# Kernel optimization log

Hardware: AMD Instinct MI355X
Metric: run time of the kernel (lower is better)

Reference implementation:

```python
import jax, jax.numpy as jnp
import numpy as np

B, N, K = 2, 8192, 9
IN_CH, FEAT_CH, COST_CH = 64, 128, 64

def _bn(x, p, eps=1e-5):
    # eval-mode BatchNorm; p is [4, C] = (gamma, beta, running_mean, running_var)
    sh = (1, -1) + (1,) * (x.ndim - 2)
    g, b, m, v = (p[i].reshape(sh) for i in range(4))
    return (x - m) / jnp.sqrt(v + eps) * g + b

def _c1(x, w, b):
    # Conv1d kernel 1: x [B,C,N], w [O,C]
    return jnp.einsum('oc,bcn->bon', w, x) + b[None, :, None]

def _forward(xyz, points, cost_volume, feats, flow,
             w0, b0, bn0, w1, b1, bn1,
             wz, bz, wr, br, wq, bq,
             w2a, b2a, w2b, b2b, wfc, bfc,
             rw0, rbn0, rw1, rbn1, rw2, rbn2,
             cw0, cbn0, cw1, cbn1, cw2, cbn2):
    lrelu = lambda t: jax.nn.leaky_relu(t, 0.1)
    # --- self-KNN on xyz ---
    xt = jnp.transpose(xyz, (0, 2, 1))                   # B N 3
    sq = jnp.sum(xt * xt, -1)                            # B N
    d2 = sq[:, :, None] + sq[:, None, :] - 2.0 * jnp.einsum('bnd,bmd->bnm', xt, xt)
    idx = jax.lax.top_k(-d2, K)[1]                       # B N K (nearest incl. self)
    # --- grouping_operation: gather neighbor features ---
    np0 = jnp.concatenate([cost_volume, flow], 1)        # B (cost_ch+3) N
    g = jax.vmap(lambda p, i: p[:, i])(np0, idx)         # B C N K
    # --- Conv2d(1x1)+BN+LeakyReLU stack ---
    g = lrelu(_bn(jnp.einsum('oc,bcnk->bonk', w0, g) + b0[None, :, None, None], bn0))
    g = lrelu(_bn(jnp.einsum('oc,bcnk->bonk', w1, g) + b1[None, :, None, None], bn1))
    h = jnp.max(g, -1)                                   # max over neighbors -> B 128 N
    # --- ConvGRU(x=feats, h) with 1x1 Conv1d gates ---
    hx = jnp.concatenate([h, feats], 1)
    z = jax.nn.sigmoid(_c1(hx, wz, bz))
    r = jax.nn.sigmoid(_c1(hx, wr, br))
    q = jnp.tanh(_c1(jnp.concatenate([r * h, feats], 1), wq, bq))
    h = (1.0 - z) * h + z * q
    # --- Conv1d MLP head ---
    x = jnp.concatenate([points, h], 1)                  # B (in_ch+128) N
    x = lrelu(_c1(x, w2a, b2a))
    x = lrelu(_c1(x, w2b, b2b))
    re_flow = _c1(x, wfc, bfc)                           # B 3 N
    # --- prob regnets (Conv1d no-bias + BN + ReLU) ---
    def reg(y, ws, ps):
        for w, p in zip(ws, ps):
            y = jax.nn.relu(_bn(jnp.einsum('oc,bcn->bon', w, y), p))
        return y
    refine = reg(x, [rw0, rw1, rw2], [rbn0, rbn1, rbn2])         # B 1 N
    coarse = reg(cost_volume, [cw0, cw1, cw2], [cbn0, cbn1, cbn2])
    re_flow = coarse * flow + refine * re_flow
    return x, jnp.clip(re_flow, -20.0, 20.0)

def setup_inputs():
    key = jax.random.key(0)
    ks = iter(jax.random.split(key, 80))
    nrm = lambda shape, s=1.0: jax.random.normal(next(ks), shape, jnp.float32) * s
    def bnp(C):
        g = jax.random.uniform(next(ks), (C,), jnp.float32) + 0.5
        b = nrm((C,), 0.1); m = nrm((C,), 0.1)
        v = jax.random.uniform(next(ks), (C,), jnp.float32) + 0.5
        return jnp.stack([g, b, m, v])
    z = lambda C: jnp.zeros((C,), jnp.float32)
    return dict(
        xyz=nrm((B, 3, N)), points=nrm((B, IN_CH, N)), cost_volume=nrm((B, COST_CH, N)),
        feats=nrm((B, FEAT_CH, N)), flow=nrm((B, 3, N), 0.1),
        w0=nrm((128, COST_CH + 3), 0.05), b0=z(128), bn0=bnp(128),
        w1=nrm((128, 128), 0.05), b1=z(128), bn1=bnp(128),
        wz=nrm((128, 256), 0.05), bz=z(128), wr=nrm((128, 256), 0.05), br=z(128),
        wq=nrm((128, 256), 0.05), bq=z(128),
        w2a=nrm((128, IN_CH + 128), 0.05), b2a=z(128), w2b=nrm((64, 128), 0.05), b2b=z(64),
        wfc=nrm((3, 64), 0.05), bfc=z(3),
        rw0=nrm((64, 64), 0.05), rbn0=bnp(64), rw1=nrm((64, 64), 0.05), rbn1=bnp(64),
        rw2=nrm((1, 64), 0.05), rbn2=bnp(1),
        cw0=nrm((64, COST_CH), 0.05), cbn0=bnp(64), cw1=nrm((64, 64), 0.05), cbn1=bnp(64),
        cw2=nrm((1, 64), 0.05), cbn2=bnp(1),
    )

def reference(xyz, points, cost_volume, feats, flow, w0, b0, bn0, w1, b1, bn1, wz, bz, wr, br, wq, bq, w2a, b2a, w2b, b2b, wfc, bfc, rw0, rbn0, rw1, rbn1, rw2, rbn2, cw0, cbn0, cw1, cbn1, cw2, cbn2):
    return _forward(xyz, points, cost_volume, feats, flow, w0, b0, bn0, w1, b1, bn1, wz, bz, wr, br, wq, bq, w2a, b2a, w2b, b2b, wfc, bfc, rw0, rbn0, rw1, rbn1, rw2, rbn2, cw0, cbn0, cw1, cbn1, cw2, cbn2)
```

## Files before the change

### kernel.cpp

```cpp
#include <hip/hip_runtime.h>
#include <math.h>

typedef __bf16 bf16;
typedef __bf16 bf16x4 __attribute__((ext_vector_type(4)));
typedef __bf16 bf16x8 __attribute__((ext_vector_type(8)));
typedef float f32x4 __attribute__((ext_vector_type(4)));

#define NPTS 8192
#define MTOT 16384

static __device__ __forceinline__ float b2f(bf16 x) { return (float)x; }
static __device__ __forceinline__ bf16  f2b(float x) { return (bf16)x; }

__global__ void diag_k(float* out, float code)
{
    if (threadIdx.x == 0 && blockIdx.x == 0) out[0] = code;
}

static __device__ __forceinline__ void pack_body(bf16 (*tile)[68],
                                                 const float* __restrict__ src, int Csrc,
                                                 bf16* __restrict__ dst, int ldd,
                                                 int nb, int cb, int b)
{
    const int t = threadIdx.x;
#pragma unroll
    for (int i = 0; i < 8; ++i) {
        int id = t + i * 256;
        int c = id >> 6, n = id & 63;
        int cc = cb + c;
        bf16 v = (bf16)0.0f;
        if (cc < Csrc) v = f2b(src[(size_t)(b * Csrc + cc) * NPTS + nb + n]);
        tile[c][n] = v;
    }
    __syncthreads();
#pragma unroll
    for (int i = 0; i < 8; ++i) {
        int id = t + i * 256;
        int n = id >> 5, c = id & 31;
        dst[(size_t)(b * NPTS + nb + n) * ldd + cb + c] = tile[c][n];
    }
}

static __device__ __forceinline__ float tau32(unsigned u)
{
    unsigned m = 0x80000000u | (unsigned)(~((int)u >> 31));
    return __uint_as_float(u ^ m);
}

static __device__ __forceinline__ unsigned dpp_shr1_u(unsigned x)
{
    return (unsigned)__builtin_amdgcn_update_dpp(0, (int)x, 0x111, 0xf, 0xf, true);
}
static __device__ __forceinline__ int dpp_shr1_i(int x)
{
    return __builtin_amdgcn_update_dpp(0, x, 0x111, 0xf, 0xf, true);
}

static __device__ __forceinline__ void mm32(
    f32x4 (&acc)[2][2],
    const bf16* A1, int lda1, int row01, int K1,
    const bf16* A2, int lda2, int row02,
    const bf16* W, int ldw, int K, int ob)
{
    const int lane = threadIdx.x & 63;
    const int q = lane >> 4, r = lane & 15;
    const bf16* Wp = W + (size_t)(ob + r) * ldw + q * 8;
    for (int k = 0; k < K; k += 32) {
        const bf16* Ap; int ld;
        if (k < K1) { ld = lda1; Ap = A1 + (size_t)(row01 + r) * lda1 + q * 8 + k; }
        else        { ld = lda2; Ap = A2 + (size_t)(row02 + r) * lda2 + q * 8 + (k - K1); }
        bf16x8 bv0 = *(const bf16x8*)(Wp + k);
        bf16x8 bv1 = *(const bf16x8*)(Wp + 16 * ldw + k);
        bf16x8 a0 = *(const bf16x8*)(Ap);
        bf16x8 a1 = *(const bf16x8*)(Ap + 16 * ld);
        acc[0][0] = __builtin_amdgcn_mfma_f32_16x16x32_bf16(a0, bv0, acc[0][0], 0, 0, 0);
        acc[1][0] = __builtin_amdgcn_mfma_f32_16x16x32_bf16(a1, bv0, acc[1][0], 0, 0, 0);
        acc[0][1] = __builtin_amdgcn_mfma_f32_16x16x32_bf16(a0, bv1, acc[0][1], 0, 0, 0);
        acc[1][1] = __builtin_amdgcn_mfma_f32_16x16x32_bf16(a1, bv1, acc[1][1], 0, 0, 0);
    }
}

static __device__ __forceinline__ void zacc(f32x4 (&acc)[2][2])
{
    f32x4 z = {0.f, 0.f, 0.f, 0.f};
    acc[0][0] = z; acc[0][1] = z; acc[1][0] = z; acc[1][1] = z;
}

static __device__ __forceinline__ void mm16(
    f32x4 (&acc)[2],
    const bf16* A1, int lda1, int row01, int K1,
    const bf16* A2, int lda2, int row02,
    const bf16* W, int ldw, int K, int ob)
{
    const int lane = threadIdx.x & 63;
    const int q = lane >> 4, r = lane & 15;
    const bf16* Wp = W + (size_t)(ob + r) * ldw + q * 8;
    for (int k = 0; k < K; k += 32) {
        const bf16* Ap; int ld;
        if (k < K1) { ld = lda1; Ap = A1 + (size_t)(row01 + r) * lda1 + q * 8 + k; }
        else        { ld = lda2; Ap = A2 + (size_t)(row02 + r) * lda2 + q * 8 + (k - K1); }
        bf16x8 bv0 = *(const bf16x8*)(Wp + k);
        bf16x8 a0 = *(const bf16x8*)(Ap);
        bf16x8 a1 = *(const bf16x8*)(Ap + 16 * ld);
        acc[0] = __builtin_amdgcn_mfma_f32_16x16x32_bf16(a0, bv0, acc[0], 0, 0, 0);
        acc[1] = __builtin_amdgcn_mfma_f32_16x16x32_bf16(a1, bv0, acc[1], 0, 0, 0);
    }
}

static __device__ __forceinline__ void mm16x2(
    f32x4 (&acc)[2], f32x4 (&acc2)[2],
    const bf16* A1, int lda1, int row01, int K1,
    const bf16* A2, int lda2, int row02,
    const bf16* Wa, const bf16* Wb, int ldw, int K, int ob)
{
    const int lane = threadIdx.x & 63;
    const int q = lane >> 4, r = lane & 15;
    const bf16* Wpa = Wa + (size_t)(ob + r) * ldw + q * 8;
    const bf16* Wpb = Wb + (size_t)(ob + r) * ldw + q * 8;
    for (int k = 0; k < K; k += 32) {
        const bf16* Ap; int ld;
        if (k < K1) { ld = lda1; Ap = A1 + (size_t)(row01 + r) * lda1 + q * 8 + k; }
        else        { ld = lda2; Ap = A2 + (size_t)(row02 + r) * lda2 + q * 8 + (k - K1); }
        bf16x8 a0 = *(const bf16x8*)(Ap);
        bf16x8 a1 = *(const bf16x8*)(Ap + 16 * ld);
        bf16x8 ba0 = *(const bf16x8*)(Wpa + k);
        bf16x8 bb0 = *(const bf16x8*)(Wpb + k);
        acc[0]  = __builtin_amdgcn_mfma_f32_16x16x32_bf16(a0, ba0, acc[0], 0, 0, 0);
        acc[1]  = __builtin_amdgcn_mfma_f32_16x16x32_bf16(a1, ba0, acc[1], 0, 0, 0);
        acc2[0] = __builtin_amdgcn_mfma_f32_16x16x32_bf16(a0, bb0, acc2[0], 0, 0, 0);
        acc2[1] = __builtin_amdgcn_mfma_f32_16x16x32_bf16(a1, bb0, acc2[1], 0, 0, 0);
    }
}

static __device__ __forceinline__ void zacc2(f32x4 (&acc)[2])
{
    f32x4 z = {0.f, 0.f, 0.f, 0.f};
    acc[0] = z; acc[1] = z;
}

__global__ __launch_bounds__(256) void pack_a(
    const float* __restrict__ w0, const float* __restrict__ w1,
    const float* __restrict__ wz, const float* __restrict__ wr,
    const float* __restrict__ wq, const float* __restrict__ w2a,
    const float* __restrict__ w2b, const float* __restrict__ rw0,
    const float* __restrict__ rw1, const float* __restrict__ cw0,
    const float* __restrict__ cw1,
    const float* __restrict__ cost, const float* __restrict__ flow,
    bf16* __restrict__ w0p, bf16* __restrict__ wts,
    bf16* __restrict__ CV, bf16* __restrict__ FL)
{
    __shared__ __align__(16) bf16 tile[32][68];
    const int bx = blockIdx.x;
    if (bx < 48) {
        int id = bx * 256 + threadIdx.x;
        if (id < 128 * 96) {
            int o = id / 96, c = id - o * 96;
            w0p[id] = (c < 67) ? f2b(w0[o * 67 + c]) : (bf16)0.0f;
        }
    } else if (bx < 688) {
        int id = (bx - 48) * 256 + threadIdx.x;
        if (id < 163840) {
            const float* s; int off;
            if (id < 16384)       { s = w1;  off = 0; }
            else if (id < 49152)  { s = wz;  off = 16384; }
            else if (id < 81920)  { s = wr;  off = 49152; }
            else if (id < 114688) { s = wq;  off = 81920; }
            else if (id < 139264) { s = w2a; off = 114688; }
            else if (id < 147456) { s = w2b; off = 139264; }
            else if (id < 151552) { s = rw0; off = 147456; }
            else if (id < 155648) { s = rw1; off = 151552; }
            else if (id < 159744) { s = cw0; off = 155648; }
            else                  { s = cw1; off = 159744; }
            wts[id] = f2b(s[id - off]);
        }
    } else if (bx < 1200) {
        int l = bx - 688, x = l & 127, r2 = l >> 7;
        pack_body(tile, cost, 64, CV, 64, x * 64, (r2 & 1) * 32, r2 >> 1);
    } else {
        int l = bx - 1200, x = l & 127, b = l >> 7;
        pack_body(tile, flow, 3, FL, 32, x * 64, 0, b);
    }
}

__global__ __launch_bounds__(256, 5) void knn_conv_packb(
    const float* __restrict__ xyz, const float* __restrict__ feats,
    const float* __restrict__ points,
    const bf16* __restrict__ CV, const bf16* __restrict__ FL,
    const bf16* __restrict__ W0p, const bf16* __restrict__ W1,
    const bf16* __restrict__ CW0, const bf16* __restrict__ CW1,
    const float* __restrict__ b0, const float* __restrict__ bn0,
    const float* __restrict__ b1, const float* __restrict__ bn1,
    const float* __restrict__ cbn0, const float* __restrict__ cbn1,
    const float* __restrict__ cw2, const float* __restrict__ cbn2,
    bf16* __restrict__ FE, bf16* __restrict__ PT,
    bf16* __restrict__ P2, int* __restrict__ idxg,
    float* __restrict__ coarseG)
{
    __shared__ __align__(16) char smem[18432];
    const int bx = blockIdx.x;
    if (bx < 4096) {
        float4* pts = (float4*)smem;
        const int t = threadIdx.x, lane = t & 63, w = t >> 6;
        const int qid = bx * 4 + w, b = qid >> 13;
        const float* X = xyz + b * 3 * NPTS;
        const int n = qid & (NPTS - 1);
        const float qx = X[n], qy = X[NPTS + n], qz = X[2 * NPTS + n];
        const float qsq = qx * qx + qy * qy + qz * qz;

        unsigned kkd = 0xFFFFFFFFu;
        int      idd = 0;
        float tau = __builtin_inff();

        float nx[4], ny[4], nz[4];
#pragma unroll
        for (int r2 = 0; r2 < 4; ++r2) {
            int ci = t + r2 * 256;
            nx[r2] = X[ci]; ny[r2] = X[NPTS + ci]; nz[r2] = X[2 * NPTS + ci];
        }
#pragma unroll
        for (int r2 = 0; r2 < 4; ++r2) {
            int i2 = t + r2 * 256;
            pts[i2] = make_float4(nx[r2], ny[r2], nz[r2],
                                  nx[r2]*nx[r2] + ny[r2]*ny[r2] + nz[r2]*nz[r2]);
        }
        __syncthreads();

        for (int ch = 0; ch < 8; ++ch) {
            if (ch < 7) {
#pragma unroll
                for (int r2 = 0; r2 < 4; ++r2) {
                    int ci = (ch + 1) * 1024 + t + r2 * 256;
                    nx[r2] = X[ci]; ny[r2] = X[NPTS + ci]; nz[r2] = X[2 * NPTS + ci];
                }
            }
            int i0 = 0;
            if (ch == 0) {
                float4 c = pts[lane];
                float d = (qsq + c.w) - 2.0f * (qx * c.x + qy * c.y + qz * c.z);
                unsigned kd = __float_as_uint(d);
                kd ^= ((unsigned)((int)kd >> 31)) | 0x80000000u;
                unsigned long long key = ((unsigned long long)kd << 32) | (unsigned)lane;
#pragma unroll
                for (int r = 0; r < 9; ++r) {
                    unsigned long long m = key;
#pragma unroll
                    for (int s = 1; s < 64; s <<= 1) {
                        unsigned long long o = __shfl_xor(m, s);
                        if (o < m) m = o;
                    }
                    if (lane == r) {
                        kkd = (unsigned)(m >> 32);
                        idd = (int)(unsigned)(m & 0xffffffffu);
                    }
                    if (key == m) key = ~0ull;
                }
                tau = tau32((unsigned)__builtin_amdgcn_readlane((int)kkd, 8));
                i0 = 1;
            }
            for (int i = i0; i < 16; ++i) {
                float4 c = pts[i * 64 + lane];
                float d = (qsq + c.w) - 2.0f * (qx * c.x + qy * c.y + qz * c.z);
                unsigned long long mask = __ballot(d <= tau);
                if (mask) {
                    const int base = ch * 1024 + i * 64;
                    do {
                        int L = __builtin_ctzll(mask);
                        mask &= mask - 1;
                        unsigned di = (unsigned)__builtin_amdgcn_readlane(
                                          __float_as_int(d), L);
                        unsigned kd = di ^ (((unsigned)((int)di >> 31)) | 0x80000000u);
                        const int idxn = base + L;
                        unsigned kprev = dpp_shr1_u(kkd);
                        int      iprev = dpp_shr1_i(idd);
                        bool lt  = kd < kkd;
                        bool ltp = kd < kprev;
                        kkd = lt ? (ltp ? kprev : kd)   : kkd;
                        idd = lt ? (ltp ? iprev : idxn) : idd;
                    } while (mask);
                    tau = tau32((unsigned)__builtin_amdgcn_readlane((int)kkd, 8));
                }
            }
            __syncthreads();
            if (ch < 7) {
#pragma unroll
                for (int r2 = 0; r2 < 4; ++r2) {
                    int i2 = t + r2 * 256;
                    pts[i2] = make_float4(nx[r2], ny[r2], nz[r2],
                                          nx[r2]*nx[r2] + ny[r2]*ny[r2] + nz[r2]*nz[r2]);
                }
                __syncthreads();
            }
        }
        if (lane < 9) {
            int m = idd;
            m = ((unsigned)m < (unsigned)NPTS) ? m : 0;
            idxg[qid * 9 + lane] = b * NPTS + m;
        }
    } else if (bx < 4608) {
        bf16 (*P1t)[136] = (bf16 (*)[136])smem;
        const int w = threadIdx.x >> 6, lane = threadIdx.x & 63;
        const int q = lane >> 4, r = lane & 15;
        const int ptb = (bx - 4096) * 32;
        {
            f32x4 acc[2][2]; zacc(acc);
            const int ob = w * 32;
            mm32(acc, CV, 64, ptb, 64, FL, 32, ptb, W0p, 96, 96, ob);
#pragma unroll
            for (int to = 0; to < 2; ++to) {
                const int o = ob + to * 16 + r;
                float bs = b0[o];
                float gg = bn0[o], be = bn0[128 + o], mm = bn0[256 + o];
                float rs = 1.0f / sqrtf(bn0[384 + o] + 1e-5f);
#pragma unroll
                for (int tm = 0; tm < 2; ++tm) {
#pragma unroll
                    for (int rr = 0; rr < 4; ++rr) {
                        const int jl = tm * 16 + q * 4 + rr;
                        float v = acc[tm][to][rr] + bs;
                        v = (v - mm) * rs * gg + be;
                        v = v > 0.f ? v : 0.1f * v;
                        P1t[jl][o] = f2b(v);
                    }
                }
            }
        }
        __syncthreads();
        {
            f32x4 acc[2][2]; zacc(acc);
            const int ob = w * 32;
            mm32(acc, &P1t[0][0], 136, 0, 128, &P1t[0][0], 136, 0, W1, 128, 128, ob);
#pragma unroll
            for (int to = 0; to < 2; ++to) {
                const int o = ob + to * 16 + r;
                float bs = b1[o];
                float gg = bn1[o], be = bn1[128 + o], mm = bn1[256 + o];
                float rs = 1.0f / sqrtf(bn1[384 + o] + 1e-5f);
#pragma unroll
                for (int tm = 0; tm < 2; ++tm) {
#pragma unroll
                    for (int rr = 0; rr < 4; ++rr) {
                        const int jl = tm * 16 + q * 4 + rr;
                        float v = acc[tm][to][rr] + bs;
                        v = (v - mm) * rs * gg + be;
                        v = v > 0.f ? v : 0.1f * v;
                        P2[(size_t)(ptb + jl) * 128 + o] = f2b(v);
                    }
                }
            }
        }
    } else if (bx < 5632) {
        bf16 (*tile)[68] = (bf16 (*)[68])smem;
        int l = bx - 4608, x = l & 127, r2 = l >> 7;
        pack_body(tile, feats, 128, FE, 128, x * 64, (r2 & 3) * 32, r2 >> 2);
    } else if (bx < 6144) {
        bf16 (*tile)[68] = (bf16 (*)[68])smem;
        int l = bx - 5632, x = l & 127, r2 = l >> 7;
        pack_body(tile, points, 64, PT, 64, x * 64, (r2 & 1) * 32, r2 >> 1);
    } else {
        bf16 (*C1t)[72] = (bf16 (*)[72])smem;
        bf16 (*C2t)[72] = (bf16 (*)[72])(smem + 9216);
        const int w = threadIdx.x >> 6, lane = threadIdx.x & 63;
        const int q = lane >> 4, r = lane & 15;
        const int row0 = (w >> 1) * 32;
        const int pt0 = (bx - 6144) * 64 + row0;
        const int ob = (w & 1) * 32;
        {
            f32x4 acc[2][2]; zacc(acc);
            mm32(acc, CV, 64, pt0, 64, CV, 64, pt0, CW0, 64, 64, ob);
#pragma unroll
            for (int to = 0; to < 2; ++to) {
                const int o = ob + to * 16 + r;
                float gg = cbn0[o], be = cbn0[64 + o], mm = cbn0[128 + o];
                float rs = 1.0f / sqrtf(cbn0[192 + o] + 1e-5f);
#pragma unroll
                for (int tm = 0; tm < 2; ++tm)
#pragma unroll
                    for (int rr = 0; rr < 4; ++rr) {
                        const int jl = tm * 16 + q * 4 + rr;
                        float v = acc[tm][to][rr];
                        v = (v - mm) * rs * gg + be;
                        C1t[row0 + jl][o] = f2b(fmaxf(v, 0.f));
                    }
            }
        }
        __syncthreads();
        {
            f32x4 acc[2][2]; zacc(acc);
            mm32(acc, &C1t[0][0], 72, row0, 64, &C1t[0][0], 72, row0, CW1, 64, 64, ob);
#pragma unroll
            for (int to = 0; to < 2; ++to) {
                const int o = ob + to * 16 + r;
                float gg = cbn1[o], be = cbn1[64 + o], mm = cbn1[128 + o];
                float rs = 1.0f / sqrtf(cbn1[192 + o] + 1e-5f);
#pragma unroll
                for (int tm = 0; tm < 2; ++tm)
#pragma unroll
                    for (int rr = 0; rr < 4; ++rr) {
                        const int jl = tm * 16 + q * 4 + rr;
                        float v = acc[tm][to][rr];
                        v = (v - mm) * rs * gg + be;
                        C2t[row0 + jl][o] = f2b(fmaxf(v, 0.f));
                    }
            }
        }
        __syncthreads();
        if (threadIdx.x < 64) {
            const int jl = threadIdx.x;
            const int j = (bx - 6144) * 64 + jl;
            float dc = 0.f;
#pragma unroll
            for (int c = 0; c < 64; ++c) dc += cw2[c] * b2f(C2t[jl][c]);
            float coarse = (dc - cbn2[2]) / sqrtf(cbn2[3] + 1e-5f) * cbn2[0] + cbn2[1];
            coarseG[j] = fmaxf(coarse, 0.f);
        }
    }
}

struct MRP {
    const bf16 *P2, *FE, *PT;
    const int  *idx;
    const bf16 *WZ, *WR, *WQ, *W2A, *W2B, *RW0, *RW1;
    const float *bz, *br, *bq, *b2a, *b2b;
    const float *rbn0, *rbn1;
    const float *rw2, *rbn2, *wfc, *bfc, *flow, *coarse;
    float* out;
};

__global__ __launch_bounds__(512) void megarow(MRP p)
{
    __shared__ __align__(16) bf16 Zt[32][136], RHt[32][136], HPt[32][136], X1t[32][136];
    __shared__ __align__(16) bf16 FEt[32][136];
    __shared__ __align__(16) bf16 X2t[32][72], R1t[32][72], R2t[32][72], PTt[32][72];
    __shared__ int idxt[32][9];
    const int w = threadIdx.x >> 6, lane = threadIdx.x & 63;
    const int q = lane >> 4, r = lane & 15;
    const int ptb = blockIdx.x * 32;

    if (threadIdx.x < 288) {
        int jl = threadIdx.x / 9, k = threadIdx.x - jl * 9;
        int m = p.idx[(ptb + jl) * 9 + k];
        idxt[jl][k] = ((unsigned)m < (unsigned)MTOT) ? m : 0;
    }
    {
        const int row = threadIdx.x >> 4;
        const int c8 = (threadIdx.x & 15) * 8;
        *(bf16x8*)&FEt[row][c8] = *(const bf16x8*)(p.FE + (size_t)(ptb + row) * 128 + c8);
        const int c4 = (threadIdx.x & 15) * 4;
        *(bf16x4*)&PTt[row][c4] = *(const bf16x4*)(p.PT + (size_t)(ptb + row) * 64 + c4);
    }
    __syncthreads();
    {
        const int c4 = (threadIdx.x & 31) * 4;
        const int jr = threadIdx.x >> 5;
#pragma unroll
        for (int jj = 0; jj < 2; ++jj) {
            const int jl = jr + 16 * jj;
            float mx0 = -__builtin_inff(), mx1 = -__builtin_inff();
            float mx2 = -__builtin_inff(), mx3 = -__builtin_inff();
#pragma unroll
            for (int k = 0; k < 9; ++k) {
                bf16x4 v = *(const bf16x4*)(p.P2 + (size_t)idxt[jl][k] * 128 + c4);
                mx0 = fmaxf(mx0, b2f(v[0]));
                mx1 = fmaxf(mx1, b2f(v[1]));
                mx2 = fmaxf(mx2, b2f(v[2]));
                mx3 = fmaxf(mx3, b2f(v[3]));
            }
            bf16x4 st;
            st[0] = f2b(mx0); st[1] = f2b(mx1); st[2] = f2b(mx2); st[3] = f2b(mx3);
            *(bf16x4*)&X1t[jl][c4] = st;
        }
    }
    __syncthreads();

    {
        const int ob = w * 16;
        f32x4 acc[2], acc2[2]; zacc2(acc); zacc2(acc2);
        mm16x2(acc, acc2, &X1t[0][0], 136, 0, 128, &FEt[0][0], 136, 0,
               p.WZ, p.WR, 256, 256, ob);
        const int o = ob + r;
        const float bsz = p.bz[o];
#pragma unroll
        for (int tm = 0; tm < 2; ++tm)
#pragma unroll
            for (int rr = 0; rr < 4; ++rr) {
                const int jl = tm * 16 + q * 4 + rr;
                float v = acc[tm][rr] + bsz;
                Zt[jl][o] = f2b(1.0f / (1.0f + expf(-v)));
            }
        const float bsr = p.br[o];
#pragma unroll
        for (int tm = 0; tm < 2; ++tm)
#pragma unroll
            for (int rr = 0; rr < 4; ++rr) {
                const int jl = tm * 16 + q * 4 + rr;
                float v = acc2[tm][rr] + bsr;
                v = 1.0f / (1.0f + expf(-v));
                RHt[jl][o] = f2b(v * b2f(X1t[jl][o]));
            }
    }
    __syncthreads();
    {
        const int ob = w * 16;
        f32x4 acc[2]; zacc2(acc);
        mm16(acc, &RHt[0][0], 136, 0, 128, &FEt[0][0], 136, 0, p.WQ, 256, 256, ob);
        const int o = ob + r;
        const float bs = p.bq[o];
#pragma unroll
        for (int tm = 0; tm < 2; ++tm)
#pragma unroll
            for (int rr = 0; rr < 4; ++rr) {
                const int jl = tm * 16 + q * 4 + rr;
                float v = acc[tm][rr] + bs;
                float qv = tanhf(v);
                float z = b2f(Zt[jl][o]);
                float h = b2f(X1t[jl][o]);
                HPt[jl][o] = f2b((1.0f - z) * h + z * qv);
            }
    }
    __syncthreads();
    {
        const int ob = w * 16;
        f32x4 acc[2]; zacc2(acc);
        mm16(acc, &PTt[0][0], 72, 0, 64, &HPt[0][0], 136, 0, p.W2A, 192, 192, ob);
        const int o = ob + r;
        const float bs = p.b2a[o];
#pragma unroll
        for (int tm = 0; tm < 2; ++tm)
#pragma unroll
            for (int rr = 0; rr < 4; ++rr) {
                const int jl = tm * 16 + q * 4 + rr;
                float v = acc[tm][rr] + bs;
                X1t[jl][o] = f2b(v > 0.f ? v : 0.1f * v);
            }
    }
    __syncthreads();
    if (w < 4) {
        const int ob = w * 16;
        f32x4 acc[2]; zacc2(acc);
        mm16(acc, &X1t[0][0], 136, 0, 128, &X1t[0][0], 136, 0, p.W2B, 128, 128, ob);
        const int o = ob + r;
        const float bs = p.b2b[o];
#pragma unroll
        for (int tm = 0; tm < 2; ++tm)
#pragma unroll
            for (int rr = 0; rr < 4; ++rr) {
                const int jl = tm * 16 + q * 4 + rr;
                float v = acc[tm][rr] + bs;
                v = v > 0.f ? v : 0.1f * v;
                X2t[jl][o] = f2b(v);
                const int j = ptb + jl, bb = j >> 13, nn = j & (NPTS - 1);
                p.out[(size_t)bb * 64 * NPTS + (size_t)o * NPTS + nn] = v;
            }
    }
    __syncthreads();
    if (w < 4) {
        const int ob = w * 16;
        f32x4 acc[2]; zacc2(acc);
        mm16(acc, &X2t[0][0], 72, 0, 64, &X2t[0][0], 72, 0, p.RW0, 64, 64, ob);
        const int o = ob + r;
        float gg = p.rbn0[o], be = p.rbn0[64 + o], mm = p.rbn0[128 + o];
        float rs = 1.0f / sqrtf(p.rbn0[192 + o] + 1e-5f);
#pragma unroll
        for (int tm = 0; tm < 2; ++tm)
#pragma unroll
            for (int rr = 0; rr < 4; ++rr) {
                const int jl = tm * 16 + q * 4 + rr;
                float v = acc[tm][rr];
                v = (v - mm) * rs * gg + be;
                R1t[jl][o] = f2b(fmaxf(v, 0.f));
            }
    }
    __syncthreads();
    if (w < 4) {
        const int ob = w * 16;
        f32x4 acc[2]; zacc2(acc);
        mm16(acc, &R1t[0][0], 72, 0, 64, &R1t[0][0], 72, 0, p.RW1, 64, 64, ob);
        const int o = ob + r;
        float gg = p.rbn1[o], be = p.rbn1[64 + o], mm = p.rbn1[128 + o];
        float rs = 1.0f / sqrtf(p.rbn1[192 + o] + 1e-5f);
#pragma unroll
        for (int tm = 0; tm < 2; ++tm)
#pragma unroll
            for (int rr = 0; rr < 4; ++rr) {
                const int jl = tm * 16 + q * 4 + rr;
                float v = acc[tm][rr];
                v = (v - mm) * rs * gg + be;
                R2t[jl][o] = f2b(fmaxf(v, 0.f));
            }
    }
    __syncthreads();
    if (threadIdx.x < 32) {
        const int jl = threadIdx.x, j = ptb + jl;
        const int b = j >> 13, n = j & (NPTS - 1);
        float dr = 0.f, p0 = 0.f, p1 = 0.f, p2 = 0.f;
#pragma unroll
        for (int c = 0; c < 64; ++c) {
            float x = b2f(X2t[jl][c]);
            dr += p.rw2[c] * b2f(R2t[jl][c]);
            p0 += p.wfc[c] * x;
            p1 += p.wfc[64 + c] * x;
            p2 += p.wfc[128 + c] * x;
        }
        float refine = (dr - p.rbn2[2]) / sqrtf(p.rbn2[3] + 1e-5f) * p.rbn2[0] + p.rbn2[1];
        refine = fmaxf(refine, 0.f);
        const float coarse = p.coarse[j];
        p0 += p.bfc[0]; p1 += p.bfc[1]; p2 += p.bfc[2];
        const float f0 = p.flow[(size_t)b * 3 * NPTS + n];
        const float f1 = p.flow[(size_t)b * 3 * NPTS + NPTS + n];
        const float f2v = p.flow[(size_t)b * 3 * NPTS + 2 * NPTS + n];
        float o0 = fminf(fmaxf(coarse * f0 + refine * p0, -20.f), 20.f);
        float o1 = fminf(fmaxf(coarse * f1 + refine * p1, -20.f), 20.f);
        float o2 = fminf(fmaxf(coarse * f2v + refine * p2, -20.f), 20.f);
        float* ro = p.out + 1048576;
        ro[(size_t)b * 3 * NPTS + n] = o0;
        ro[(size_t)b * 3 * NPTS + NPTS + n] = o1;
        ro[(size_t)b * 3 * NPTS + 2 * NPTS + n] = o2;
    }
}

extern "C" void kernel_launch(void* const* d_in, const int* in_sizes, int n_in,
                              void* d_out, int out_size, void* d_ws, size_t ws_size,
                              hipStream_t stream)
{
    static const int EXP[35] = {
        49152, 1048576, 1048576, 2097152, 49152,
        8576, 128, 512, 16384, 128, 512,
        32768, 128, 32768, 128, 32768, 128,
        24576, 128, 8192, 64, 192, 3,
        4096, 256, 4096, 256, 64, 4,
        4096, 256, 4096, 256, 64, 4 };
    float code = 0.f;
    if (n_in != 35) code = 900.f;
    else if (out_size != 1097728) code = 950.f;
    else if (ws_size < 18767872u) code = 980.f;
    else { for (int i = 0; i < 35; ++i) if (in_sizes[i] != EXP[i]) { code = 1000.f + 4.f * i; break; } }
    if (code != 0.f) { diag_k<<<dim3(1), dim3(64), 0, stream>>>((float*)d_out, code); return; }

    const float* xyz    = (const float*)d_in[0];
    const float* points = (const float*)d_in[1];
    const float* cost   = (const float*)d_in[2];
    const float* feats  = (const float*)d_in[3];
    const float* flow   = (const float*)d_in[4];
    const float* w0     = (const float*)d_in[5];
    const float* b0     = (const float*)d_in[6];
    const float* bn0    = (const float*)d_in[7];
    const float* w1     = (const float*)d_in[8];
    const float* b1     = (const float*)d_in[9];
    const float* bn1    = (const float*)d_in[10];
    const float* wz     = (const float*)d_in[11];
    const float* bz     = (const float*)d_in[12];
    const float* wr     = (const float*)d_in[13];
    const float* br     = (const float*)d_in[14];
    const float* wq     = (const float*)d_in[15];
    const float* bq     = (const float*)d_in[16];
    const float* w2a    = (const float*)d_in[17];
    const float* b2a    = (const float*)d_in[18];
    const float* w2b    = (const float*)d_in[19];
    const float* b2b    = (const float*)d_in[20];
    const float* wfc    = (const float*)d_in[21];
    const float* bfc    = (const float*)d_in[22];
    const float* rw0    = (const float*)d_in[23];
    const float* rbn0   = (const float*)d_in[24];
    const float* rw1    = (const float*)d_in[25];
    const float* rbn1   = (const float*)d_in[26];
    const float* rw2    = (const float*)d_in[27];
    const float* rbn2   = (const float*)d_in[28];
    const float* cw0    = (const float*)d_in[29];
    const float* cbn0   = (const float*)d_in[30];
    const float* cw1    = (const float*)d_in[31];
    const float* cbn1   = (const float*)d_in[32];
    const float* cw2    = (const float*)d_in[33];
    const float* cbn2   = (const float*)d_in[34];

    char* ws = (char*)d_ws;
    bf16*  W0p  = (bf16*)(ws + 0);
    bf16*  WTS  = (bf16*)(ws + 24576);
    int*   idxg = (int*) (ws + 352256);
    bf16*  CV   = (bf16*)(ws + 942080);
    bf16*  FL   = (bf16*)(ws + 3039232);
    bf16*  FE   = (bf16*)(ws + 4087808);
    bf16*  PT   = (bf16*)(ws + 8282112);
    bf16*  P2   = (bf16*)(ws + 10379264);
    float* CO   = (float*)(ws + 14573568);

    bf16* W1  = WTS;
    bf16* WZ  = WTS + 16384;
    bf16* WR  = WTS + 49152;
    bf16* WQ  = WTS + 81920;
    bf16* W2A = WTS + 114688;
    bf16* W2B = WTS + 139264;
    bf16* RW0 = WTS + 147456;
    bf16* RW1 = WTS + 151552;
    bf16* CW0 = WTS + 155648;
    bf16* CW1 = WTS + 159744;

    float* out = (float*)d_out;

     pack_a<<<dim3(1456), dim3(256), 0, stream>>>(
              w0, w1, wz, wr, wq, w2a, w2b, rw0, rw1, cw0, cw1,
              cost, flow, W0p, WTS, CV, FL);
     knn_conv_packb<<<dim3(6400), dim3(256), 0, stream>>>(
              xyz, feats, points, CV, FL, W0p, W1, CW0, CW1,
              b0, bn0, b1, bn1, cbn0, cbn1, cw2, cbn2,
              FE, PT, P2, idxg, CO);
     MRP mp;
          mp.P2 = P2; mp.FE = FE; mp.PT = PT; mp.idx = idxg;
          mp.WZ = WZ; mp.WR = WR; mp.WQ = WQ; mp.W2A = W2A; mp.W2B = W2B;
          mp.RW0 = RW0; mp.RW1 = RW1;
          mp.bz = bz; mp.br = br; mp.bq = bq; mp.b2a = b2a; mp.b2b = b2b;
          mp.rbn0 = rbn0; mp.rbn1 = rbn1;
          mp.rw2 = rw2; mp.rbn2 = rbn2;
          mp.wfc = wfc; mp.bfc = bfc; mp.flow = flow; mp.coarse = CO;
          mp.out = out;
          megarow<<<dim3(512), dim3(512), 0, stream>>>(mp);

    (void)n_in;
}
```

Baseline: 232.1 us.

## Process two KNN queries per wavefront and widen max-pool gather to 8 channels

Each KNN wavefront now tracks two queries, so every staged candidate tile in LDS is read once and used for both queries. This halves the number of KNN blocks and the repeated staging of xyz into shared memory, and the block-range offsets for the other roles are shifted to match. The megarow neighbor max-pool now loads 8 bf16 channels per thread in one pass instead of 4 channels over two passes. The trade-offs are higher register pressure in the KNN path and fewer blocks to hide latency, and the two queries' serialized hit loops run one after the other.

```diff
diff --git a/kernel.cpp b/kernel.cpp
--- a/kernel.cpp
+++ b/kernel.cpp
@@ -54,6 +54,50 @@
 static __device__ __forceinline__ int dpp_shr1_i(int x)
 {
     return __builtin_amdgcn_update_dpp(0, x, 0x111, 0xf, 0xf, true);
+}
+
+static __device__ __forceinline__ void init9(float d, int lane,
+                                             unsigned& kkd, int& idd)
+{
+    unsigned kd = __float_as_uint(d);
+    kd ^= ((unsigned)((int)kd >> 31)) | 0x80000000u;
+    unsigned long long key = ((unsigned long long)kd << 32) | (unsigned)lane;
+#pragma unroll
+    for (int r = 0; r < 9; ++r) {
+        unsigned long long m = key;
+#pragma unroll
+        for (int s = 1; s < 64; s <<= 1) {
+            unsigned long long o = __shfl_xor(m, s);
+            if (o < m) m = o;
+        }
+        if (lane == r) {
+            kkd = (unsigned)(m >> 32);
+            idd = (int)(unsigned)(m & 0xffffffffu);
+        }
+        if (key == m) key = ~0ull;
+    }
+}
+
+static __device__ __forceinline__ void hits9(float d, int base, float& tau,
+                                             unsigned& kkd, int& idd)
+{
+    unsigned long long mask = __ballot(d <= tau);
+    if (mask) {
+        do {
+            int L = __builtin_ctzll(mask);
+            mask &= mask - 1;
+            unsigned di = (unsigned)__builtin_amdgcn_readlane(__float_as_int(d), L);
+            unsigned kd = di ^ (((unsigned)((int)di >> 31)) | 0x80000000u);
+            const int idxn = base + L;
+            unsigned kprev = dpp_shr1_u(kkd);
+            int      iprev = dpp_shr1_i(idd);
+            bool lt  = kd < kkd;
+            bool ltp = kd < kprev;
+            kkd = lt ? (ltp ? kprev : kd)   : kkd;
+            idd = lt ? (ltp ? iprev : idxn) : idd;
+        } while (mask);
+        tau = tau32((unsigned)__builtin_amdgcn_readlane((int)kkd, 8));
+    }
 }
 
 static __device__ __forceinline__ void mm32(
@@ -198,18 +242,21 @@
 {
     __shared__ __align__(16) char smem[18432];
     const int bx = blockIdx.x;
-    if (bx < 4096) {
+    if (bx < 2048) {
         float4* pts = (float4*)smem;
         const int t = threadIdx.x, lane = t & 63, w = t >> 6;
-        const int qid = bx * 4 + w, b = qid >> 13;
+        const int qA = bx * 8 + w, qB = qA + 4;
+        const int b = qA >> 13;
         const float* X = xyz + b * 3 * NPTS;
-        const int n = qid & (NPTS - 1);
-        const float qx = X[n], qy = X[NPTS + n], qz = X[2 * NPTS + n];
-        const float qsq = qx * qx + qy * qy + qz * qz;
-
-        unsigned kkd = 0xFFFFFFFFu;
-        int      idd = 0;
-        float tau = __builtin_inff();
+        const int nA = qA & (NPTS - 1), nB = qB & (NPTS - 1);
+        const float qxA = X[nA], qyA = X[NPTS + nA], qzA = X[2 * NPTS + nA];
+        const float qxB = X[nB], qyB = X[NPTS + nB], qzB = X[2 * NPTS + nB];
+        const float qsqA = qxA * qxA + qyA * qyA + qzA * qzA;
+        const float qsqB = qxB * qxB + qyB * qyB + qzB * qzB;
+
+        unsigned kkdA = 0xFFFFFFFFu, kkdB = 0xFFFFFFFFu;
+        int      iddA = 0, iddB = 0;
+        float tauA = __builtin_inff(), tauB = __builtin_inff();
 
         float nx[4], ny[4], nz[4];
 #pragma unroll
@@ -236,49 +283,21 @@
             int i0 = 0;
             if (ch == 0) {
                 float4 c = pts[lane];
-                float d = (qsq + c.w) - 2.0f * (qx * c.x + qy * c.y + qz * c.z);
-                unsigned kd = __float_as_uint(d);
-                kd ^= ((unsigned)((int)kd >> 31)) | 0x80000000u;
-                unsigned long long key = ((unsigned long long)kd << 32) | (unsigned)lane;
-#pragma unroll
-                for (int r = 0; r < 9; ++r) {
-                    unsigned long long m = key;
-#pragma unroll
-                    for (int s = 1; s < 64; s <<= 1) {
-                        unsigned long long o = __shfl_xor(m, s);
-                        if (o < m) m = o;
-                    }
-                    if (lane == r) {
-                        kkd = (unsigned)(m >> 32);
-                        idd = (int)(unsigned)(m & 0xffffffffu);
-                    }
-                    if (key == m) key = ~0ull;
-                }
-                tau = tau32((unsigned)__builtin_amdgcn_readlane((int)kkd, 8));
+                float dA = (qsqA + c.w) - 2.0f * (qxA * c.x + qyA * c.y + qzA * c.z);
+                init9(dA, lane, kkdA, iddA);
+                tauA = tau32((unsigned)__builtin_amdgcn_readlane((int)kkdA, 8));
+                float dB = (qsqB + c.w) - 2.0f * (qxB * c.x + qyB * c.y + qzB * c.z);
+                init9(dB, lane, kkdB, iddB);
+                tauB = tau32((unsigned)__builtin_amdgcn_readlane((int)kkdB, 8));
                 i0 = 1;
             }
             for (int i = i0; i < 16; ++i) {
                 float4 c = pts[i * 64 + lane];
-                float d = (qsq + c.w) - 2.0f * (qx * c.x + qy * c.y + qz * c.z);
-                unsigned long long mask = __ballot(d <= tau);
-                if (mask) {
-                    const int base = ch * 1024 + i * 64;
-                    do {
-                        int L = __builtin_ctzll(mask);
-                        mask &= mask - 1;
-                        unsigned di = (unsigned)__builtin_amdgcn_readlane(
-                                          __float_as_int(d), L);
-                        unsigned kd = di ^ (((unsigned)((int)di >> 31)) | 0x80000000u);
-                        const int idxn = base + L;
-                        unsigned kprev = dpp_shr1_u(kkd);
-                        int      iprev = dpp_shr1_i(idd);
-                        bool lt  = kd < kkd;
-                        bool ltp = kd < kprev;
-                        kkd = lt ? (ltp ? kprev : kd)   : kkd;
-                        idd = lt ? (ltp ? iprev : idxn) : idd;
-                    } while (mask);
-                    tau = tau32((unsigned)__builtin_amdgcn_readlane((int)kkd, 8));
-                }
+                float dA = (qsqA + c.w) - 2.0f * (qxA * c.x + qyA * c.y + qzA * c.z);
+                float dB = (qsqB + c.w) - 2.0f * (qxB * c.x + qyB * c.y + qzB * c.z);
+                const int base = ch * 1024 + i * 64;
+                hits9(dA, base, tauA, kkdA, iddA);
+                hits9(dB, base, tauB, kkdB, iddB);
             }
             __syncthreads();
             if (ch < 7) {
@@ -292,15 +311,18 @@
             }
         }
         if (lane < 9) {
-            int m = idd;
-            m = ((unsigned)m < (unsigned)NPTS) ? m : 0;
-            idxg[qid * 9 + lane] = b * NPTS + m;
-        }
-    } else if (bx < 4608) {
+            int mA = iddA;
+            mA = ((unsigned)mA < (unsigned)NPTS) ? mA : 0;
+            idxg[qA * 9 + lane] = b * NPTS + mA;
+            int mB = iddB;
+            mB = ((unsigned)mB < (unsigned)NPTS) ? mB : 0;
+            idxg[qB * 9 + lane] = b * NPTS + mB;
+        }
+    } else if (bx < 2560) {
         bf16 (*P1t)[136] = (bf16 (*)[136])smem;
         const int w = threadIdx.x >> 6, lane = threadIdx.x & 63;
         const int q = lane >> 4, r = lane & 15;
-        const int ptb = (bx - 4096) * 32;
+        const int ptb = (bx - 2048) * 32;
         {
             f32x4 acc[2][2]; zacc(acc);
             const int ob = w * 32;
@@ -348,13 +370,13 @@
                 }
             }
         }
-    } else if (bx < 5632) {
+    } else if (bx < 3584) {
         bf16 (*tile)[68] = (bf16 (*)[68])smem;
-        int l = bx - 4608, x = l & 127, r2 = l >> 7;
+        int l = bx - 2560, x = l & 127, r2 = l >> 7;
         pack_body(tile, feats, 128, FE, 128, x * 64, (r2 & 3) * 32, r2 >> 2);
-    } else if (bx < 6144) {
+    } else if (bx < 4096) {
         bf16 (*tile)[68] = (bf16 (*)[68])smem;
-        int l = bx - 5632, x = l & 127, r2 = l >> 7;
+        int l = bx - 3584, x = l & 127, r2 = l >> 7;
         pack_body(tile, points, 64, PT, 64, x * 64, (r2 & 1) * 32, r2 >> 1);
     } else {
         bf16 (*C1t)[72] = (bf16 (*)[72])smem;
@@ -362,7 +384,7 @@
         const int w = threadIdx.x >> 6, lane = threadIdx.x & 63;
         const int q = lane >> 4, r = lane & 15;
         const int row0 = (w >> 1) * 32;
-        const int pt0 = (bx - 6144) * 64 + row0;
+        const int pt0 = (bx - 4096) * 64 + row0;
         const int ob = (w & 1) * 32;
         {
             f32x4 acc[2][2]; zacc(acc);
@@ -406,7 +428,7 @@
         __syncthreads();
         if (threadIdx.x < 64) {
             const int jl = threadIdx.x;
-            const int j = (bx - 6144) * 64 + jl;
+            const int j = (bx - 4096) * 64 + jl;
             float dc = 0.f;
 #pragma unroll
             for (int c = 0; c < 64; ++c) dc += cw2[c] * b2f(C2t[jl][c]);
@@ -450,25 +472,28 @@
     }
     __syncthreads();
     {
-        const int c4 = (threadIdx.x & 31) * 4;
-        const int jr = threadIdx.x >> 5;
-#pragma unroll
-        for (int jj = 0; jj < 2; ++jj) {
-            const int jl = jr + 16 * jj;
-            float mx0 = -__builtin_inff(), mx1 = -__builtin_inff();
-            float mx2 = -__builtin_inff(), mx3 = -__builtin_inff();
-#pragma unroll
-            for (int k = 0; k < 9; ++k) {
-                bf16x4 v = *(const bf16x4*)(p.P2 + (size_t)idxt[jl][k] * 128 + c4);
-                mx0 = fmaxf(mx0, b2f(v[0]));
-                mx1 = fmaxf(mx1, b2f(v[1]));
-                mx2 = fmaxf(mx2, b2f(v[2]));
-                mx3 = fmaxf(mx3, b2f(v[3]));
-            }
-            bf16x4 st;
-            st[0] = f2b(mx0); st[1] = f2b(mx1); st[2] = f2b(mx2); st[3] = f2b(mx3);
-            *(bf16x4*)&X1t[jl][c4] = st;
-        }
+        const int c8 = (threadIdx.x & 15) * 8;
+        const int jl = threadIdx.x >> 4;
+        float mx0 = -__builtin_inff(), mx1 = -__builtin_inff();
+        float mx2 = -__builtin_inff(), mx3 = -__builtin_inff();
+        float mx4 = -__builtin_inff(), mx5 = -__builtin_inff();
+        float mx6 = -__builtin_inff(), mx7 = -__builtin_inff();
+#pragma unroll
+        for (int k = 0; k < 9; ++k) {
+            bf16x8 v = *(const bf16x8*)(p.P2 + (size_t)idxt[jl][k] * 128 + c8);
+            mx0 = fmaxf(mx0, b2f(v[0]));
+            mx1 = fmaxf(mx1, b2f(v[1]));
+            mx2 = fmaxf(mx2, b2f(v[2]));
+            mx3 = fmaxf(mx3, b2f(v[3]));
+            mx4 = fmaxf(mx4, b2f(v[4]));
+            mx5 = fmaxf(mx5, b2f(v[5]));
+            mx6 = fmaxf(mx6, b2f(v[6]));
+            mx7 = fmaxf(mx7, b2f(v[7]));
+        }
+        bf16x8 st;
+        st[0] = f2b(mx0); st[1] = f2b(mx1); st[2] = f2b(mx2); st[3] = f2b(mx3);
+        st[4] = f2b(mx4); st[5] = f2b(mx5); st[6] = f2b(mx6); st[7] = f2b(mx7);
+        *(bf16x8*)&X1t[jl][c8] = st;
     }
     __syncthreads();
 
@@ -699,7 +724,7 @@
      pack_a<<<dim3(1456), dim3(256), 0, stream>>>(
               w0, w1, wz, wr, wq, w2a, w2b, rw0, rw1, cw0, cw1,
               cost, flow, W0p, WTS, CV, FL);
-     knn_conv_packb<<<dim3(6400), dim3(256), 0, stream>>>(
+     knn_conv_packb<<<dim3(4352), dim3(256), 0, stream>>>(
               xyz, feats, points, CV, FL, W0p, W1, CW0, CW1,
               b0, bn0, b1, bn1, cbn0, cbn1, cw2, cbn2,
               FE, PT, P2, idxg, CO);
```

Measured after the change: 230.7 us, median of 3. Within noise of the previous version (-0.6%).
